# Kernel tuning notes

Measured on AMD Instinct MI355X. Metric: run time of the kernel, lower is better.

Reference implementation:

```python
import jax, jax.numpy as jnp
import numpy as np

K_CORR = 2048        # num_correspondences (init kwarg)
MAX_CORR = 8192      # static pad size for the variable-length nonzero output
THRES_START = 0.5
THRES_STEP = 0.01


def setup_inputs() -> dict:
    key = jax.random.key(0)
    k1, k2, k3 = jax.random.split(key, 3)
    N = M = 8193  # 8192 superpoints + 1 dustbin
    # shift so exp(scores) is mostly well below the 0.5 starting threshold,
    # making the iterative threshold search actually iterate (as in practice
    # with log-domain OT scores)
    matching_scores = jax.random.normal(k1, (N, M), dtype=jnp.float32) - 5.0
    ref_n2p_scores_c = jax.random.uniform(k2, (N - 1,), dtype=jnp.float32)
    src_n2p_scores_c = jax.random.uniform(k3, (M - 1,), dtype=jnp.float32)
    return {
        "matching_scores": matching_scores,
        "ref_n2p_scores_c": ref_n2p_scores_c,
        "src_n2p_scores_c": src_n2p_scores_c,
    }


def _find_thres(inner, k):
    """Replicates: while count(score[:-1,:-1] > thres) < k: thres -= 0.01."""
    def cond(t):
        return jnp.sum(inner > t) < k
    def body(t):
        return t - jnp.float32(THRES_STEP)
    return jax.lax.while_loop(cond, body, jnp.float32(THRES_START))


def reference(matching_scores, ref_n2p_scores_c, src_n2p_scores_c):
    s = jnp.exp(matching_scores)
    # n2p reweighting of the non-dustbin block, as in the torch in-place update
    inner = s[:-1, :-1] * (ref_n2p_scores_c[:, None] * src_n2p_scores_c[None, :])
    # threshold search is discrete -> not differentiated
    thres = _find_thres(jax.lax.stop_gradient(inner), K_CORR)
    mask = inner > thres
    count = jnp.sum(mask)
    # torch returns variable-length nonzero in row-major order; we pad to MAX_CORR
    r, c = jnp.nonzero(mask, size=MAX_CORR, fill_value=0)
    valid = jnp.arange(MAX_CORR) < count
    corr_scores = jnp.where(valid, inner[r, c], 0.0)
    ref_corr_indices = jnp.where(valid, r, -1)
    src_corr_indices = jnp.where(valid, c, -1)
    return ref_corr_indices, src_corr_indices, corr_scores
```

## Files before the change

kernel.cpp:

```cpp
#include <hip/hip_runtime.h>

#define NROWS 8192
#define NCOLS 8192
#define LD    8193
#define NBINS 64
#define KCORR 2048
#define MAXC  8192
#define CAP   192
#define RPB   4
#define FCUT_LOG (-2.5257286443082556f)

__device__ __forceinline__ float inner_val(float m, float rr, float sc) {
    float p = rr * sc;
    return expf(m) * p;
}

__device__ __forceinline__ void wave_thres(const unsigned* __restrict__ hist,
                                           float* th_out, int* ns_out) {
    int lane = threadIdx.x & 63;
    unsigned cum = hist[lane];
    #pragma unroll
    for (int off = 1; off < 64; off <<= 1) {
        unsigned u = __shfl_up(cum, off);
        if (lane >= off) cum += u;
    }
    unsigned long long mk = __ballot(cum >= (unsigned)KCORR);
    int nsel = mk ? (int)(__ffsll((unsigned long long)mk) - 1) : (NBINS - 1);
    float tv = 0.5f;
    for (int n = 0; n < nsel; ++n) tv = tv - 0.01f;
    *th_out = tv;
    *ns_out = nsel;
}

__global__ void init_kernel(float* __restrict__ out, unsigned* __restrict__ hist,
                            unsigned* __restrict__ ovfl) {
    int i = blockIdx.x * blockDim.x + threadIdx.x;
    if (i < 2 * MAXC)       out[i] = -1.0f;
    else if (i < 3 * MAXC)  out[i] = 0.0f;
    if (i < NBINS) hist[i] = 0u;
    if (i == NBINS) *ovfl = 0u;
}

__global__ __launch_bounds__(256, 2) void hist_kernel(
    const float* __restrict__ ms, const float* __restrict__ refs,
    const float* __restrict__ srcs, unsigned* __restrict__ hist,
    unsigned* __restrict__ candcnt, unsigned* __restrict__ cand_col,
    float* __restrict__ cand_v, unsigned* __restrict__ ovfl, int use_cand)
{
    __shared__ float t[NBINS];
    __shared__ unsigned sub[NBINS];
    __shared__ unsigned cnt[RPB];
    __shared__ uint2 pairs[RPB * CAP];
    int tid = threadIdx.x;
    if (tid == 0) {
        float tv = 0.5f;
        for (int n = 0; n < NBINS; ++n) { t[n] = tv; tv = tv - 0.01f; }
    }
    if (tid < NBINS) sub[tid] = 0u;
    if (tid < RPB) cnt[tid] = 0u;
    __syncthreads();

    int r0 = blockIdx.x * RPB;

    auto push = [&](int r, int col, float m) {
        unsigned slot = atomicAdd(&cnt[r], 1u);
        if (slot < CAP)
            pairs[r * CAP + slot] = make_uint2((unsigned)col, __float_as_uint(m));
    };

#define ISSUE(b, R0, R1, R2, R3) do {                                          \
        constexpr int r_ = (b) >> 1, h_ = (b) & 1;                             \
        int row_ = r0 + r_;                                                    \
        int s_ = (4 - (row_ & 3)) & 3;              \
        const float4* p4_ = (const float4*)(ms + (size_t)row_ * LD + s_);      \
        int i0_ = h_ * 1024 + tid;                                             \
        R0 = p4_[i0_];                                                         \
        R1 = p4_[i0_ + 256];                                                   \
        R2 = p4_[i0_ + 512];                                                   \
        if (h_ == 1) {                                                         \
            int nb_ = (NCOLS - s_) >> 2;              \
            if (i0_ + 768 < nb_) R3 = p4_[i0_ + 768];                          \
            else R3 = make_float4(-1e30f, -1e30f, -1e30f, -1e30f);             \
        } else {                                                               \
            R3 = p4_[i0_ + 768];                                               \
        }                                                                      \
    } while (0)

#define PROC(r_, c0_, q_) do {                                                 \
        bool a0 = (q_).x > FCUT_LOG, a1 = (q_).y > FCUT_LOG;                   \
        bool a2 = (q_).z > FCUT_LOG, a3 = (q_).w > FCUT_LOG;                   \
        if (a0 | a1 | a2 | a3) {                    \
            if (a0) push(r_, (c0_) + 0, (q_).x);                               \
            if (a1) push(r_, (c0_) + 1, (q_).y);                               \
            if (a2) push(r_, (c0_) + 2, (q_).z);                               \
            if (a3) push(r_, (c0_) + 3, (q_).w);                               \
        }                                                                      \
    } while (0)

#define CONSUME(b, R0, R1, R2, R3) do {                                        \
        constexpr int r_ = (b) >> 1, h_ = (b) & 1;                             \
        int s_ = (4 - ((r0 + r_) & 3)) & 3;                                    \
        int cb_ = s_ + 4 * (h_ * 1024 + tid);                                  \
        PROC(r_, cb_ + 0,    R0);                                              \
        PROC(r_, cb_ + 1024, R1);                                              \
        PROC(r_, cb_ + 2048, R2);                                              \
        PROC(r_, cb_ + 3072, R3);                                              \
    } while (0)

    float4 A0, A1, A2, A3, B0, B1, B2, B3, C0, C1, C2, C3;
    ISSUE(0, A0, A1, A2, A3);
    ISSUE(1, B0, B1, B2, B3);
    ISSUE(2, C0, C1, C2, C3);
    CONSUME(0, A0, A1, A2, A3);
    ISSUE(3, A0, A1, A2, A3);
    CONSUME(1, B0, B1, B2, B3);
    ISSUE(4, B0, B1, B2, B3);
    CONSUME(2, C0, C1, C2, C3);
    ISSUE(5, C0, C1, C2, C3);
    CONSUME(3, A0, A1, A2, A3);
    ISSUE(6, A0, A1, A2, A3);
    CONSUME(4, B0, B1, B2, B3);
    ISSUE(7, B0, B1, B2, B3);
    CONSUME(5, C0, C1, C2, C3);
    CONSUME(6, A0, A1, A2, A3);
    CONSUME(7, B0, B1, B2, B3);

#undef ISSUE
#undef PROC
#undef CONSUME

    if (tid < RPB * 8) {
        int r = tid >> 3, e = tid & 7;
        int row = r0 + r;
        int s = (4 - (row & 3)) & 3;
        int nb = (NCOLS - s) >> 2;
        int done = s + 4 * nb;
        int col = -1;
        if (e < s) col = e;
        else if (e - s < NCOLS - done) col = done + (e - s);
        if (col >= 0) {
            float m = ms[(size_t)row * LD + col];
            if (m > FCUT_LOG) push(r, col, m);
        }
    }
    __syncthreads();

    for (int r = 0; r < RPB; ++r) {
        int row = r0 + r;
        unsigned C = cnt[r];
        unsigned Cc = (C < CAP) ? C : CAP;
        float rr = refs[row];
        for (unsigned i = tid; i < Cc; i += 256) {
            uint2 pr = pairs[r * CAP + i];
            int col = (int)pr.x;
            float m = __uint_as_float(pr.y);
            float v = inner_val(m, rr, srcs[col]);
            int g = (int)floorf((0.5f - v) * 100.0f) + 1;
            g = (g < 0) ? 0 : ((g > NBINS) ? NBINS : g);
            while (g < NBINS && t[g] >= v) ++g;
            while (g > 0 && t[g - 1] < v) --g;
            atomicAdd(&sub[g], 1u);
            if (use_cand) {
                cand_col[(size_t)row * CAP + i] = (unsigned)col;
                cand_v[(size_t)row * CAP + i]   = v;
            }
        }
        if (tid == 0) {
            if (use_cand) candcnt[row] = C;
            if (C > CAP) atomicOr(ovfl, 1u);
        }
    }
    __syncthreads();

    if (tid < 64) {
        unsigned v = sub[tid];
        unsigned p = v;
        #pragma unroll
        for (int off = 1; off < 64; off <<= 1) {
            unsigned u = __shfl_up(p, off);
            if (tid >= off) p += u;
        }
        unsigned binned = __shfl(p, 63);
        unsigned g = (tid == 63) ? (v + (unsigned)(RPB * NCOLS) - binned) : v;
        if (g) atomicAdd(&hist[tid], g);
    }
}

__global__ __launch_bounds__(256) void count_kernel(
    const float* __restrict__ ms, const float* __restrict__ refs,
    const float* __restrict__ srcs, const unsigned* __restrict__ hist,
    const unsigned* __restrict__ ovfl, const unsigned* __restrict__ candcnt,
    const float* __restrict__ cand_v, unsigned* __restrict__ rowcnt,
    int use_cand)
{
    __shared__ unsigned tot;
    float th; int ns;
    wave_thres(hist, &th, &ns);
    bool fast = (use_cand && ns <= 41 && *ovfl == 0u);

    if (fast) {
        int tid = threadIdx.x, wv = tid >> 6, lane = tid & 63;
        int row = blockIdx.x * 4 + wv;
        unsigned C = candcnt[row];
        unsigned c = 0;
        if (C <= CAP) {
            const float* cv = cand_v + (size_t)row * CAP;
            for (unsigned i = lane; i < C; i += 64)
                c += (cv[i] > th) ? 1u : 0u;
        } else {
            float rr = refs[row];
            const float* mrow = ms + (size_t)row * LD;
            for (int col = lane; col < NCOLS; col += 64)
                c += (inner_val(mrow[col], rr, srcs[col]) > th) ? 1u : 0u;
        }
        #pragma unroll
        for (int off = 32; off > 0; off >>= 1) c += __shfl_down(c, off);
        if (lane == 0) rowcnt[row] = c;
        return;
    }

    for (int r4 = 0; r4 < 4; ++r4) {
        int row = blockIdx.x * 4 + r4;
        if (threadIdx.x == 0) tot = 0;
        __syncthreads();
        float rr = refs[row];
        const float* mrow = ms + (size_t)row * LD;
        unsigned c = 0;
        for (int col = threadIdx.x; col < NCOLS; col += 256)
            c += (inner_val(mrow[col], rr, srcs[col]) > th) ? 1u : 0u;
        atomicAdd(&tot, c);
        __syncthreads();
        if (threadIdx.x == 0) rowcnt[row] = tot;
        __syncthreads();
    }
}

__global__ __launch_bounds__(1024) void scan_kernel(
    const unsigned* __restrict__ rowcnt, unsigned* __restrict__ rowoff)
{
    __shared__ unsigned wsum[16];
    int tid = threadIdx.x, lane = tid & 63, wv = tid >> 6;
    int r0 = tid * 8;
    unsigned c[8], s = 0;
    #pragma unroll
    for (int k = 0; k < 8; ++k) { c[k] = rowcnt[r0 + k]; s += c[k]; }
    unsigned p = s;
    #pragma unroll
    for (int off = 1; off < 64; off <<= 1) {
        unsigned u = __shfl_up(p, off);
        if (lane >= off) p += u;
    }
    if (lane == 63) wsum[wv] = p;
    __syncthreads();
    if (wv == 0 && lane < 16) {
        unsigned w = wsum[lane];
        #pragma unroll
        for (int off = 1; off < 16; off <<= 1) {
            unsigned u = __shfl_up(w, off);
            if (lane >= off) w += u;
        }
        wsum[lane] = w;
    }
    __syncthreads();
    unsigned excl = (wv > 0 ? wsum[wv - 1] : 0u) + (p - s);
    #pragma unroll
    for (int k = 0; k < 8; ++k) { rowoff[r0 + k] = excl; excl += c[k]; }
    if (tid == 1023) rowoff[NROWS] = excl;
}

__global__ __launch_bounds__(256) void cwrite_kernel(
    const float* __restrict__ ms, const float* __restrict__ refs,
    const float* __restrict__ srcs, const unsigned* __restrict__ hist,
    const unsigned* __restrict__ ovfl, const unsigned* __restrict__ rowoff,
    const unsigned* __restrict__ candcnt, const unsigned* __restrict__ cand_col,
    const float* __restrict__ cand_v, float* __restrict__ out, int use_cand)
{
    __shared__ unsigned s_col[4][64];
    __shared__ float    s_val[4][64];
    int tid = threadIdx.x, wv = tid >> 6, lane = tid & 63;
    int row = blockIdx.x * 4 + wv;
    unsigned base = rowoff[row], next = rowoff[row + 1];
    if (base == next || base >= MAXC) return;
    float th; int ns;
    wave_thres(hist, &th, &ns);
    unsigned k = next - base;
    bool full = (!use_cand) || (ns >= 42) || (*ovfl != 0u) ||
                (candcnt[row] > CAP) || (k > 64);

    if (!full) {
        unsigned C = candcnt[row];
        const unsigned* cc = cand_col + (size_t)row * CAP;
        const float*    cv = cand_v  + (size_t)row * CAP;
        unsigned nrun = 0;
        for (unsigned c0 = 0; c0 < C; c0 += 64) {
            unsigned i = c0 + lane;
            bool sel = false; unsigned col = 0; float v = 0.f;
            if (i < C) { col = cc[i]; v = cv[i]; sel = (v > th); }
            unsigned long long mk = __ballot(sel);
            if (sel) {
                unsigned idx = nrun + (unsigned)__popcll(mk & ((1ull << lane) - 1ull));
                if (idx < 64) { s_col[wv][idx] = col; s_val[wv][idx] = v; }
            }
            nrun += (unsigned)__popcll(mk);
        }
        __builtin_amdgcn_s_waitcnt(0);
        __builtin_amdgcn_wave_barrier();
        unsigned kk = (nrun < k) ? nrun : k;
        if (kk > 64) kk = 64;
        if (lane < (int)kk) {
            unsigned mycol = s_col[wv][lane];
            float    myval = s_val[wv][lane];
            unsigned rank = 0;
            for (unsigned j = 0; j < kk; ++j)
                rank += (s_col[wv][j] < mycol) ? 1u : 0u;
            unsigned pos = base + rank;
            if (pos < MAXC) {
                out[pos]            = (float)row;
                out[MAXC + pos]     = (float)mycol;
                out[2 * MAXC + pos] = myval;
            }
        }
        return;
    }

    float rr = refs[row];
    const float* mrow = ms + (size_t)row * LD;
    unsigned running = base;
    for (int c0 = 0; c0 < NCOLS && running < next && running < MAXC; c0 += 64) {
        int col = c0 + lane;
        float v = inner_val(mrow[col], rr, srcs[col]);
        bool pred = v > th;
        unsigned long long mk = __ballot(pred);
        if (pred) {
            unsigned pos = running + (unsigned)__popcll(mk & ((1ull << lane) - 1ull));
            if (pos < MAXC) {
                out[pos]            = (float)row;
                out[MAXC + pos]     = (float)col;
                out[2 * MAXC + pos] = v;
            }
        }
        running += (unsigned)__popcll(mk);
    }
}

extern "C" void kernel_launch(void* const* d_in, const int* in_sizes, int n_in,
                              void* d_out, int out_size, void* d_ws, size_t ws_size,
                              hipStream_t stream) {
    const float* ms  = (const float*)d_in[0];
    const float* ref = (const float*)d_in[1];
    const float* src = (const float*)d_in[2];
    float* out = (float*)d_out;

    char* w = (char*)d_ws;
    unsigned* hist   = (unsigned*)(w);
    unsigned* ovfl   = (unsigned*)(w + 264);
    unsigned* rowcnt = (unsigned*)(w + 512);
    unsigned* rowoff = (unsigned*)(w + 512 + NROWS * 4);
    size_t cc_off = 512 + (size_t)NROWS * 4 + (size_t)(NROWS + 1) * 4;
    cc_off = (cc_off + 255) & ~(size_t)255;
    unsigned* candcnt  = (unsigned*)(w + cc_off);
    size_t col_off = cc_off + (size_t)NROWS * 4;
    unsigned* cand_col = (unsigned*)(w + col_off);
    size_t cv_off = col_off + (size_t)NROWS * CAP * 4;
    float* cand_v      = (float*)(w + cv_off);
    size_t end_off = cv_off + (size_t)NROWS * CAP * 4;

    int use_cand = (ws_size >= end_off) ? 1 : 0;

    init_kernel<<<96, 256, 0, stream>>>(out, hist, ovfl);
    hist_kernel<<<NROWS / RPB, 256, 0, stream>>>(ms, ref, src, hist, candcnt,
                                                 cand_col, cand_v, ovfl, use_cand);
    count_kernel<<<NROWS / 4, 256, 0, stream>>>(ms, ref, src, hist, ovfl,
                                                candcnt, cand_v, rowcnt, use_cand);
    scan_kernel<<<1, 1024, 0, stream>>>(rowcnt, rowoff);
    cwrite_kernel<<<NROWS / 4, 256, 0, stream>>>(ms, ref, src, hist, ovfl,
                                                 rowoff, candcnt, cand_col,
                                                 cand_v, out, use_cand);
}
```

Measured before the change: 380.6 us.

## Fuse count, scan and compaction into one cooperative kernel with grid sync

Replaces the count, single-block scan and compaction-write kernels with one cooperative kernel. Each block counts 8 rows and writes per-row counts, then a grid-wide sync lets every block redundantly prefix-sum all row counts to get its own offsets, and finally it writes its compacted rows. The aim is to cut two kernel launches and the serial one-block scan. In exchange it adds a grid barrier, redundant scan work in every block and a co-residency requirement for 1024 blocks, with the old three-kernel path kept as a fallback if the cooperative launch fails.

```diff
diff --git a/kernel.cpp b/kernel.cpp
--- a/kernel.cpp
+++ b/kernel.cpp
@@ -1,4 +1,5 @@
 #include <hip/hip_runtime.h>
+#include <hip/hip_cooperative_groups.h>
 
 #define NROWS 8192
 #define NCOLS 8192
@@ -186,6 +187,134 @@
     }
 }
 
+__global__ __launch_bounds__(256, 4) void tail_kernel(
+    const float* __restrict__ ms, const float* __restrict__ refs,
+    const float* __restrict__ srcs, const unsigned* __restrict__ hist,
+    const unsigned* __restrict__ ovfl, const unsigned* __restrict__ candcnt,
+    const unsigned* __restrict__ cand_col, const float* __restrict__ cand_v,
+    unsigned* __restrict__ rowcnt, float* __restrict__ out, int use_cand)
+{
+    __shared__ unsigned wpart[4];
+    __shared__ unsigned rowo[9];
+    __shared__ unsigned s_col[4][64];
+    __shared__ float    s_val[4][64];
+
+    int tid = threadIdx.x, wv = tid >> 6, lane = tid & 63;
+    int b = blockIdx.x;
+    float th; int ns;
+    wave_thres(hist, &th, &ns);
+    bool fast = (use_cand && ns <= 41 && *ovfl == 0u);
+
+    for (int lr = wv; lr < 8; lr += 4) {
+        int row = b * 8 + lr;
+        unsigned C = fast ? candcnt[row] : (CAP + 1u);
+        unsigned c = 0;
+        if (fast && C <= CAP) {
+            const float* cv = cand_v + (size_t)row * CAP;
+            for (unsigned i = lane; i < C; i += 64)
+                c += (cv[i] > th) ? 1u : 0u;
+        } else {
+            float rr = refs[row];
+            const float* mrow = ms + (size_t)row * LD;
+            for (int col = lane; col < NCOLS; col += 64)
+                c += (inner_val(mrow[col], rr, srcs[col]) > th) ? 1u : 0u;
+        }
+        #pragma unroll
+        for (int off = 32; off > 0; off >>= 1) c += __shfl_down(c, off);
+        if (lane == 0) rowcnt[row] = c;
+    }
+    __threadfence();
+    cooperative_groups::this_grid().sync();
+
+    unsigned s = 0;
+    int base32 = tid << 5;
+    for (int k2 = 0; k2 < 32; ++k2) s += rowcnt[base32 + k2];
+    unsigned p = s;
+    #pragma unroll
+    for (int off = 1; off < 64; off <<= 1) {
+        unsigned u = __shfl_up(p, off);
+        if (lane >= off) p += u;
+    }
+    if (lane == 63) wpart[wv] = p;
+    __syncthreads();
+    unsigned wbase = 0;
+    for (int j = 0; j < wv; ++j) wbase += wpart[j];
+    int tstar = b >> 2;
+    int o = (b & 3) << 3;
+    if (tid == tstar) {
+        unsigned e = wbase + p - s;
+        for (int k2 = 0; k2 < o; ++k2) e += rowcnt[(tstar << 5) + k2];
+        #pragma unroll
+        for (int j = 0; j < 8; ++j) { rowo[j] = e; e += rowcnt[b * 8 + j]; }
+        rowo[8] = e;
+    }
+    __syncthreads();
+
+    for (int lr = wv; lr < 8; lr += 4) {
+        int row = b * 8 + lr;
+        unsigned base = rowo[lr], next = rowo[lr + 1];
+        if (base == next || base >= MAXC) continue;
+        unsigned k = next - base;
+        bool fullp = (!fast) || (candcnt[row] > CAP) || (k > 64);
+
+        if (!fullp) {
+            unsigned C = candcnt[row];
+            const unsigned* cc = cand_col + (size_t)row * CAP;
+            const float*    cv = cand_v  + (size_t)row * CAP;
+            unsigned nrun = 0;
+            for (unsigned c0 = 0; c0 < C; c0 += 64) {
+                unsigned i = c0 + lane;
+                bool sel = false; unsigned col = 0; float v = 0.f;
+                if (i < C) { col = cc[i]; v = cv[i]; sel = (v > th); }
+                unsigned long long mk = __ballot(sel);
+                if (sel) {
+                    unsigned idx = nrun + (unsigned)__popcll(mk & ((1ull << lane) - 1ull));
+                    if (idx < 64) { s_col[wv][idx] = col; s_val[wv][idx] = v; }
+                }
+                nrun += (unsigned)__popcll(mk);
+            }
+            __builtin_amdgcn_s_waitcnt(0);
+            __builtin_amdgcn_wave_barrier();
+            unsigned kk = (nrun < k) ? nrun : k;
+            if (kk > 64) kk = 64;
+            if (lane < (int)kk) {
+                unsigned mycol = s_col[wv][lane];
+                float    myval = s_val[wv][lane];
+                unsigned rank = 0;
+                for (unsigned j = 0; j < kk; ++j)
+                    rank += (s_col[wv][j] < mycol) ? 1u : 0u;
+                unsigned pos = base + rank;
+                if (pos < MAXC) {
+                    out[pos]            = (float)row;
+                    out[MAXC + pos]     = (float)mycol;
+                    out[2 * MAXC + pos] = myval;
+                }
+            }
+        } else {
+            float rr = refs[row];
+            const float* mrow = ms + (size_t)row * LD;
+            unsigned running = base;
+            for (int c0 = 0; c0 < NCOLS && running < next && running < MAXC; c0 += 64) {
+                int col = c0 + lane;
+                float v = inner_val(mrow[col], rr, srcs[col]);
+                bool pred = v > th;
+                unsigned long long mk = __ballot(pred);
+                if (pred) {
+                    unsigned pos = running + (unsigned)__popcll(mk & ((1ull << lane) - 1ull));
+                    if (pos < MAXC) {
+                        out[pos]            = (float)row;
+                        out[MAXC + pos]     = (float)col;
+                        out[2 * MAXC + pos] = v;
+                    }
+                }
+                running += (unsigned)__popcll(mk);
+            }
+        }
+        __builtin_amdgcn_s_waitcnt(0);
+        __builtin_amdgcn_wave_barrier();
+    }
+}
+
 __global__ __launch_bounds__(256) void count_kernel(
     const float* __restrict__ ms, const float* __restrict__ refs,
     const float* __restrict__ srcs, const unsigned* __restrict__ hist,
@@ -370,10 +499,22 @@
     init_kernel<<<96, 256, 0, stream>>>(out, hist, ovfl);
     hist_kernel<<<NROWS / RPB, 256, 0, stream>>>(ms, ref, src, hist, candcnt,
                                                  cand_col, cand_v, ovfl, use_cand);
-    count_kernel<<<NROWS / 4, 256, 0, stream>>>(ms, ref, src, hist, ovfl,
-                                                candcnt, cand_v, rowcnt, use_cand);
-    scan_kernel<<<1, 1024, 0, stream>>>(rowcnt, rowoff);
-    cwrite_kernel<<<NROWS / 4, 256, 0, stream>>>(ms, ref, src, hist, ovfl,
-                                                 rowoff, candcnt, cand_col,
-                                                 cand_v, out, use_cand);
-}
+
+    void* kargs[] = {
+        (void*)&ms, (void*)&ref, (void*)&src, (void*)&hist, (void*)&ovfl,
+        (void*)&candcnt, (void*)&cand_col, (void*)&cand_v,
+        (void*)&rowcnt, (void*)&out, (void*)&use_cand
+    };
+    hipError_t ce = hipLaunchCooperativeKernel((const void*)tail_kernel,
+                                               dim3(NROWS / 8), dim3(256),
+                                               kargs, 0, stream);
+    if (ce != hipSuccess) {
+        count_kernel<<<NROWS / 4, 256, 0, stream>>>(ms, ref, src, hist, ovfl,
+                                                    candcnt, cand_v, rowcnt,
+                                                    use_cand);
+        scan_kernel<<<1, 1024, 0, stream>>>(rowcnt, rowoff);
+        cwrite_kernel<<<NROWS / 4, 256, 0, stream>>>(ms, ref, src, hist, ovfl,
+                                                     rowoff, candcnt, cand_col,
+                                                     cand_v, out, use_cand);
+    }
+}
```

New measurement: 502.4 us. 1.32x slower.
